# Performance work log

Measured on AMD Instinct MI355X. Metric: run time of the kernel, lower is better.

Reference implementation:

```python
import jax, jax.numpy as jnp
import numpy as np

B, C, W, H = 16, 512, 64, 64
OUT, NH = 512, 8
HD = OUT // NH          # 64
K = 64                  # kernel_size == attended axis length (height)


def setup_inputs() -> dict:
    key = jax.random.key(0)
    k0, k1, k2, k3 = jax.random.split(key, 4)
    s = float(HD) ** -0.5
    return {
        "x": jax.random.normal(k0, (B, C, W, H), jnp.float32),
        "in_proj_weight": jax.random.normal(k1, (2 * OUT, C), jnp.float32) * s,
        "in_proj_bias": jnp.zeros((2 * OUT,), jnp.float32),
        "out_proj_w": jax.random.normal(k2, (OUT, OUT), jnp.float32) * s,
        "out_proj_b": jnp.zeros((OUT,), jnp.float32),
        "relative": jax.random.normal(k3, (2 * HD, 2 * K - 1), jnp.float32) * s,
    }


def reference(x, in_proj_weight, in_proj_bias, out_proj_w, out_proj_b, relative):
    b, c, w, h = x.shape
    hd2 = HD // 2
    # width=False, self-attention path: permute(0,3,2,1) then flat view
    xq = jnp.transpose(x, (0, 3, 2, 1)).reshape(b * w, h, c)
    qkv = xq @ in_proj_weight.T + in_proj_bias
    q, k, v = jnp.split(qkv, [OUT // 2, OUT], axis=2)

    # relative position embeddings gathered into [2*HD, K, K]
    rel_idx = jnp.arange(K)[:, None] - jnp.arange(K)[None, :] + (K - 1)  # key i, query j
    emb = relative[:, rel_idx]                                          # [2*HD, K, K]
    q_emb, k_emb, v_emb = jnp.split(emb, [hd2, HD], axis=0)

    # [bw, heads, ch, pos]
    q = q.reshape(b * w, h, NH, hd2).transpose(0, 2, 3, 1)
    k = k.reshape(b * w, h, NH, hd2).transpose(0, 2, 3, 1)
    v = v.reshape(b * w, h, NH, HD).transpose(0, 2, 3, 1)

    qr = jnp.einsum('bgci,cij->bgij', q, q_emb)
    kr = jnp.einsum('bgci,cij->bgij', k, k_emb).swapaxes(2, 3)
    qk = jnp.einsum('bgci,bgcj->bgij', q, k)
    sim = jax.nn.softmax(qk + qr + kr, axis=3)

    sv = jnp.einsum('bgij,bgcj->bgci', sim, v)     # [bw, NH, HD, h]
    sve = jnp.einsum('bgij,cij->bgci', sim, v_emb)  # [bw, NH, HD, h]
    out = (sv + sve).reshape(b * w, OUT, h).swapaxes(1, 2)  # [bw, h, OUT]
    out = out @ out_proj_w.T + out_proj_b
    # [b, w, h, OUT] -> transpose(2,3) -> permute(0,2,3,1) == transpose(0,3,2,1)
    out = out.reshape(b, w, h, OUT).transpose(0, 3, 2, 1)   # [B, OUT, H, W]
    return out
```

## Files before the change

### kernel.cpp

```cpp
#include <hip/hip_runtime.h>

using u16 = unsigned short;
using u32 = unsigned int;
typedef __attribute__((ext_vector_type(8))) _Float16 h8v;
typedef __attribute__((ext_vector_type(8))) u16 us8;
typedef __attribute__((ext_vector_type(4))) float f4v;

__device__ __forceinline__ u16 f2h(float f) {
  _Float16 h = (_Float16)f;
  return __builtin_bit_cast(unsigned short, h);
}
__device__ __forceinline__ _Float16 bits2h(u16 u) {
  return __builtin_bit_cast(_Float16, u);
}

__device__ __forceinline__ f4v mfma16(h8v a, h8v b, f4v c) {
  return __builtin_amdgcn_mfma_f32_16x16x32_f16(a, b, c, 0, 0, 0);
}

__device__ __forceinline__ void gll16(const void* g, void* l) {
  __builtin_amdgcn_global_load_lds(
      (const __attribute__((address_space(1))) void*)g,
      (__attribute__((address_space(3))) void*)l, 16, 0, 0);
}


__global__ __launch_bounds__(256) void k0_setup(
    const float* __restrict__ w1, const float* __restrict__ wout,
    const float* __restrict__ rel, u16* __restrict__ W1b, u16* __restrict__ Woutb,
    u16* __restrict__ EqT, u16* __restrict__ EkT, u16* __restrict__ Evp)
{
  int idx = blockIdx.x * 256 + threadIdx.x;
  if (idx < 524288) {
    W1b[idx] = f2h(w1[idx]);
  } else if (idx < 786432) {
    int k = idx - 524288; Woutb[k] = f2h(wout[k]);
  } else if (idx < 790528) {
    int k = idx - 786432; int t = k >> 5, c = k & 31;
    EqT[k] = (t < 127) ? f2h(rel[c * 127 + t]) : (u16)0;
  } else if (idx < 794624) {
    int k = idx - 790528; int t = k >> 5, c = k & 31;
    EkT[k] = (t < 127) ? f2h(rel[(32 + c) * 127 + t]) : (u16)0;
  } else if (idx < 802816) {
    int k = idx - 794624; int c = k >> 7, t = k & 127;
    Evp[k] = (t < 127) ? f2h(rel[(64 + c) * 127 + t]) : (u16)0;
  }
}

__global__ __launch_bounds__(256) void k0t_transpose(
    const float* __restrict__ x, u16* __restrict__ xT)
{
  const int bid = blockIdx.x;
  const int cc = bid & 7, w = (bid >> 3) & 63, b = bid >> 9;
  const int c0 = cc * 64;
  const int t = threadIdx.x;
  __shared__ float T[64 * 65];

  const float* xb = x + ((size_t)(b * 512 + c0) * 64 + w) * 64;
#pragma unroll
  for (int p = 0; p < 4; p++) {
    int ci = (t >> 4) + p * 16;
    int pos = (t & 15) * 4;
    float4 v = *(const float4*)&xb[(size_t)ci * 4096 + pos];
    T[ci * 65 + pos + 0] = v.x; T[ci * 65 + pos + 1] = v.y;
    T[ci * 65 + pos + 2] = v.z; T[ci * 65 + pos + 3] = v.w;
  }
  __syncthreads();
  size_t Rb = (size_t)b * 4096 + (size_t)w * 64;
#pragma unroll
  for (int p = 0; p < 2; p++) {
    int u = p * 256 + t;
    int h = u >> 3, ch = u & 7;
    us8 o;
#pragma unroll
    for (int e = 0; e < 8; e++) o[e] = f2h(T[(ch * 8 + e) * 65 + h]);
    *(us8*)&xT[(Rb + h) * 512 + c0 + ch * 8] = o;
  }
}

__global__ __launch_bounds__(512, 1) void k1_qkv(
    const u16* __restrict__ xT, const u16* __restrict__ W1b,
    const float* __restrict__ bias, u16* __restrict__ qkv)
{
  __shared__ u16 POOL[81920];
  u16* XL = POOL;
  u16* Bl = POOL + 65536;
  const int rt = blockIdx.x;
  const int b = rt >> 5, w0 = (rt & 31) * 2;
  const int tid = threadIdx.x;
  const int l = tid & 63, wv = tid >> 6;
  const int lr = l & 15, lg = l >> 4;
  const int osub = (wv & 1) * 64;
  const int rsub = (wv >> 1) * 32;
  const size_t Rbase = (size_t)rt * 128;

#pragma unroll
  for (int i = 0; i < 16; i++) {
    int r = wv * 16 + i;
    gll16(xT + (Rbase + r) * 512 + ((l ^ (r & 7)) << 3), XL + r * 512);
  }

  auto stageB = [&](int ot, int kk, int buf) {
#pragma unroll
    for (int q = 0; q < 2; q++) {
      int slot = q * 512 + tid;
      int o = slot >> 3, c4 = slot & 7;
      gll16(W1b + (size_t)(ot * 128 + o) * 512 + kk * 64 + ((c4 ^ (o & 7)) << 3),
            Bl + buf * 8192 + slot * 8);
    }
  };

  stageB(0, 0, 0);
  __syncthreads();

  for (int ot = 0; ot < 8; ot++) {
    const int o0 = ot * 128;
    f4v acc[4][2];
#pragma unroll
    for (int mt = 0; mt < 4; mt++)
#pragma unroll
      for (int nt = 0; nt < 2; nt++) acc[mt][nt] = (f4v){0.f, 0.f, 0.f, 0.f};

#pragma unroll
    for (int kk = 0; kk < 8; kk++) {
      int cur = kk & 1;
      if (kk < 7) stageB(ot, kk + 1, cur ^ 1);
      h8v wf[4][2], xf[2][2];
#pragma unroll
      for (int mt = 0; mt < 4; mt++)
#pragma unroll
        for (int kc = 0; kc < 2; kc++) {
          int o = osub + mt * 16 + lr;
          wf[mt][kc] = *(const h8v*)&Bl[cur * 8192 + o * 64 +
                                        (((kc * 4 + lg) ^ (o & 7)) << 3)];
        }
#pragma unroll
      for (int nt = 0; nt < 2; nt++)
#pragma unroll
        for (int kc = 0; kc < 2; kc++) {
          int r = rsub + nt * 16 + lr;
          xf[nt][kc] = *(const h8v*)&XL[r * 512 + kk * 64 +
                                        (((kc * 4 + lg) ^ (r & 7)) << 3)];
        }
#pragma unroll
      for (int mt = 0; mt < 4; mt++)
#pragma unroll
        for (int nt = 0; nt < 2; nt++)
#pragma unroll
          for (int kc = 0; kc < 2; kc++)
            acc[mt][nt] = mfma16(wf[mt][kc], xf[nt][kc], acc[mt][nt]);
      __syncthreads();
    }

    u16* Tr = Bl;
#pragma unroll
    for (int mt = 0; mt < 4; mt++)
#pragma unroll
      for (int nt = 0; nt < 2; nt++) {
        int r = rsub + nt * 16 + lr;
#pragma unroll
        for (int ep = 0; ep < 2; ep++) {
          int o_ = osub + mt * 16 + lg * 4 + 2 * ep;
          float v0 = acc[mt][nt][2 * ep + 0] + bias[o0 + o_];
          float v1 = acc[mt][nt][2 * ep + 1] + bias[o0 + o_ + 1];
          unsigned pk = (unsigned)f2h(v0) | ((unsigned)f2h(v1) << 16);
          int cc = o_ >> 3;
          int dst = (cc & 8) | ((cc & 7) ^ (r & 7));
          *(unsigned*)&Tr[r * 128 + dst * 8 + (o_ & 7)] = pk;
        }
      }
    __syncthreads();
#pragma unroll
    for (int p = 0; p < 4; p++) {
      int u = p * 512 + tid;
      int r = u >> 4, cc = u & 15;
      int dst = (cc & 8) | ((cc & 7) ^ (r & 7));
      us8 v = *(const us8*)&Tr[r * 128 + dst * 8];
      int h = r & 63, wl = r >> 6;
      size_t S = (size_t)(b * 64 + h) * 64 + w0 + wl;
      *(us8*)&qkv[S * 1024 + o0 + cc * 8] = v;
    }
    __syncthreads();
    if (ot < 7) { stageB(ot + 1, 0, 0); __syncthreads(); }
  }
}

__global__ __launch_bounds__(256, 4) void k2_attn(
    const u16* __restrict__ qkv, const u16* __restrict__ EqT,
    const u16* __restrict__ EkT, const u16* __restrict__ Evp,
    u16* __restrict__ attn)
{
  const int bid = blockIdx.x;
  const int s = bid >> 3, g = bid & 7;
  const int tid = threadIdx.x;
  const int l = tid & 63, wv = tid >> 6;
  const int lr = l & 15, lg = l >> 4;
  const int i0 = wv * 16;
  const u16* base = qkv + (size_t)s * 65536;

  __shared__ __align__(16) u16 POOL[16896];
  u16* QEt  = POOL;
  u16* KEtT = POOL + 8448;
  u16* Pl   = POOL;
  u16* VTl  = POOL + 4096;
  u16* Psh  = POOL + 8192;

  us8 vreg0, vreg1;
  {
    int u0 = tid,        j0_ = u0 >> 3, cb0 = u0 & 7;
    int u1 = tid + 256,  j1_ = u1 >> 3, cb1 = u1 & 7;
    vreg0 = *(const us8*)(base + j0_ * 1024 + 512 + g * 64 + cb0 * 8);
    vreg1 = *(const us8*)(base + j1_ * 1024 + 512 + g * 64 + cb1 * 8);
  }

  h8v qf = *(const h8v*)(base + (i0 + lr) * 1024 + g * 32 + lg * 8);
  h8v kf[4];
#pragma unroll
  for (int jt = 0; jt < 4; jt++)
    kf[jt] = *(const h8v*)(base + (jt * 16 + lr) * 1024 + 256 + g * 32 + lg * 8);

  const f4v z4 = {0.f, 0.f, 0.f, 0.f};

#pragma unroll
  for (int tt = 0; tt < 8; tt++) {
    h8v eb = *(const h8v*)(EqT + (tt * 16 + lr) * 32 + lg * 8);
    f4v d = mfma16(qf, eb, z4);
#pragma unroll
    for (int p = 0; p < 2; p++) {
      u32 pk = (u32)f2h(d[2 * p]) | ((u32)f2h(d[2 * p + 1]) << 16);
      *(u32*)&QEt[(tt * 16 + lr) * 66 + i0 + lg * 4 + 2 * p] = pk;
    }
  }
#pragma unroll
  for (int q = 0; q < 2; q++) {
    int tt = wv * 2 + q;
    h8v ea = *(const h8v*)(EkT + (tt * 16 + lr) * 32 + lg * 8);
#pragma unroll
    for (int jt = 0; jt < 4; jt++) {
      f4v d = mfma16(ea, kf[jt], z4);
#pragma unroll
      for (int e = 0; e < 4; e++)
        KEtT[(tt * 16 + 4 * lg + e) * 66 + jt * 16 + lr] = f2h(d[e]);
    }
  }
  f4v sc[4];
#pragma unroll
  for (int jt = 0; jt < 4; jt++) sc[jt] = mfma16(qf, kf[jt], z4);

  __syncthreads();

  float pv[4][4];
#pragma unroll
  for (int jt = 0; jt < 4; jt++)
#pragma unroll
    for (int r = 0; r < 4; r++) {
      int i = i0 + lg * 4 + r;
      int j = jt * 16 + lr;
      int tq = i - j + 63;
      pv[jt][r] = sc[jt][r] + (float)bits2h(QEt[tq * 66 + i]) +
                  (float)bits2h(KEtT[(126 - tq) * 66 + j]);
    }
  float rsum[4];
#pragma unroll
  for (int r = 0; r < 4; r++) {
    float m = fmaxf(fmaxf(pv[0][r], pv[1][r]), fmaxf(pv[2][r], pv[3][r]));
    m = fmaxf(m, __shfl_xor(m, 1));
    m = fmaxf(m, __shfl_xor(m, 2));
    m = fmaxf(m, __shfl_xor(m, 4));
    m = fmaxf(m, __shfl_xor(m, 8));
    float t0 = 0.f;
#pragma unroll
    for (int jt = 0; jt < 4; jt++) {
      pv[jt][r] = exp2f((pv[jt][r] - m) * 1.4426950408889634f);
      t0 += pv[jt][r];
    }
    t0 += __shfl_xor(t0, 1);
    t0 += __shfl_xor(t0, 2);
    t0 += __shfl_xor(t0, 4);
    t0 += __shfl_xor(t0, 8);
    rsum[r] = t0;
  }

  __syncthreads();

#pragma unroll
  for (int jt = 0; jt < 4; jt++)
#pragma unroll
    for (int r = 0; r < 4; r++) {
      int i = i0 + lg * 4 + r;
      int j = jt * 16 + lr;
      u16 ph = f2h(pv[jt][r]);
      Pl[i * 64 + (((j >> 3) ^ (i & 7)) << 3) + (j & 7)] = ph;
      int d = i + 63 - j;
      int cd = d >> 3;
      Psh[i * 128 + (((cd & 8) | ((cd & 7) ^ (i & 7))) << 3) + (d & 7)] = ph;
    }
  {
    int zi = tid >> 2;
#pragma unroll
    for (int kk = 0; kk < 16; kk++) {
      int k = (tid & 3) * 16 + kk;
      int col = (k < zi) ? k : (k + 64);
      int cd = col >> 3;
      Psh[zi * 128 + (((cd & 8) | ((cd & 7) ^ (zi & 7))) << 3) + (col & 7)] = 0;
    }
    int u0 = tid, j0_ = u0 >> 3, cb0 = u0 & 7;
#pragma unroll
    for (int e = 0; e < 8; e++) {
      int c = cb0 * 8 + e;
      VTl[c * 64 + (((j0_ >> 3) ^ (c & 7)) << 3) + (j0_ & 7)] = (u16)vreg0[e];
    }
    int u1 = tid + 256, j1_ = u1 >> 3, cb1 = u1 & 7;
#pragma unroll
    for (int e = 0; e < 8; e++) {
      int c = cb1 * 8 + e;
      VTl[c * 64 + (((j1_ >> 3) ^ (c & 7)) << 3) + (j1_ & 7)] = (u16)vreg1[e];
    }
  }
  __syncthreads();

  f4v acc[4] = {z4, z4, z4, z4};
  {
    int i = i0 + lr;
#pragma unroll
    for (int kc = 0; kc < 2; kc++) {
      h8v pa = *(const h8v*)&Pl[i * 64 + (((kc * 4 + lg) ^ (i & 7)) << 3)];
#pragma unroll
      for (int ct = 0; ct < 4; ct++) {
        int cA = ct * 16 + lr;
        h8v vb = *(const h8v*)&VTl[cA * 64 + (((kc * 4 + lg) ^ (cA & 7)) << 3)];
        acc[ct] = mfma16(pa, vb, acc[ct]);
      }
    }
#pragma unroll
    for (int tc = 0; tc < 4; tc++) {
      int cd = tc * 4 + lg;
      int cds = (cd & 8) | ((cd & 7) ^ (i & 7));
      h8v pa = *(const h8v*)&Psh[i * 128 + cds * 8];
#pragma unroll
      for (int ct = 0; ct < 4; ct++) {
        h8v eb = *(const h8v*)(Evp + (ct * 16 + lr) * 128 + tc * 32 + lg * 8);
        acc[ct] = mfma16(pa, eb, acc[ct]);
      }
    }
  }
  float inv[4];
#pragma unroll
  for (int r = 0; r < 4; r++) inv[r] = 1.f / rsum[r];
#pragma unroll
  for (int ct = 0; ct < 4; ct++)
#pragma unroll
    for (int r = 0; r < 4; r++) {
      int i = i0 + lg * 4 + r;
      attn[(size_t)(s * 64 + i) * 512 + g * 64 + ct * 16 + lr] =
          f2h(acc[ct][r] * inv[r]);
    }
}

__global__ __launch_bounds__(512) void k3_oproj(
    const u16* __restrict__ attn, const u16* __restrict__ Woutb,
    const float* __restrict__ ob, float* __restrict__ out)
{
  const int bid = blockIdx.x;
  const int b = bid >> 6, w = bid & 63;
  const int tid = threadIdx.x;
  const int l = tid & 63, wv = tid >> 6;
  const int lr = l & 15, lg = l >> 4;

  __shared__ u16 Bl[2][64 * 64];

  f4v acc[4][4];
#pragma unroll
  for (int a_ = 0; a_ < 4; a_++)
#pragma unroll
    for (int b_ = 0; b_ < 4; b_++) acc[a_][b_] = (f4v){0.f, 0.f, 0.f, 0.f};

  auto stageB = [&](int kk, int buf) {
    int c0 = kk * 64;
    int h_l = wv * 8 + (l >> 3);
    int p = l & 7;
    const u16* src = attn + ((size_t)b * 4096 + (size_t)h_l * 64 + w) * 512 + c0 +
                     ((p ^ (h_l & 7)) << 3);
    gll16(src, &Bl[buf][wv * 512]);
  };

  stageB(0, 0);
  __syncthreads();

  for (int kk = 0; kk < 8; kk++) {
    int cur = kk & 1, nxt = cur ^ 1;
    if (kk < 7) stageB(kk + 1, nxt);
    int c0 = kk * 64;
    h8v af[4][2], bf[4][2];
#pragma unroll
    for (int mt = 0; mt < 4; mt++)
#pragma unroll
      for (int kc = 0; kc < 2; kc++)
        af[mt][kc] = *(const h8v*)(Woutb + (size_t)(wv * 64 + mt * 16 + lr) * 512 +
                                   c0 + kc * 32 + lg * 8);
#pragma unroll
    for (int jt = 0; jt < 4; jt++)
#pragma unroll
      for (int kc = 0; kc < 2; kc++) {
        int h = jt * 16 + lr;
        bf[jt][kc] = *(const h8v*)&Bl[cur][h * 64 + (((kc * 4 + lg) ^ (h & 7)) << 3)];
      }
#pragma unroll
    for (int mt = 0; mt < 4; mt++)
#pragma unroll
      for (int jt = 0; jt < 4; jt++)
#pragma unroll
        for (int kc = 0; kc < 2; kc++)
          acc[mt][jt] = mfma16(af[mt][kc], bf[jt][kc], acc[mt][jt]);
    __syncthreads();
  }

#pragma unroll
  for (int mt = 0; mt < 4; mt++)
#pragma unroll
    for (int jt = 0; jt < 4; jt++)
#pragma unroll
      for (int e = 0; e < 4; e++) {
        int o = wv * 64 + mt * 16 + lg * 4 + e;
        int h = jt * 16 + lr;
        out[(((size_t)b * 512 + o) * 64 + w) * 64 + h] = acc[mt][jt][e] + ob[o];
      }
}

extern "C" void kernel_launch(void* const* d_in, const int* in_sizes, int n_in,
                              void* d_out, int out_size, void* d_ws, size_t ws_size,
                              hipStream_t stream)
{
  (void)in_sizes; (void)n_in; (void)out_size; (void)ws_size;
  const float* x    = (const float*)d_in[0];
  const float* w1   = (const float*)d_in[1];
  const float* b1   = (const float*)d_in[2];
  const float* wout = (const float*)d_in[3];
  const float* bo   = (const float*)d_in[4];
  const float* rel  = (const float*)d_in[5];
  float* out = (float*)d_out;

  char* ws = (char*)d_ws;
  u16* qkv_ws  = (u16*)ws;
  u16* attn_ws = (u16*)(ws + 134217728);
  u16* xT_ws   = attn_ws;
  u16* W1b     = (u16*)(ws + 201326592);
  u16* Woutb   = (u16*)(ws + 202375168);
  u16* EqT     = (u16*)(ws + 202899456);
  u16* EkT     = (u16*)(ws + 202907648);
  u16* Evp     = (u16*)(ws + 202915840);

  k0_setup<<<dim3(3136), dim3(256), 0, stream>>>(w1, wout, rel, W1b, Woutb, EqT, EkT, Evp);
  k0t_transpose<<<dim3(8192), dim3(256), 0, stream>>>(x, xT_ws);
  k1_qkv  <<<dim3(512),  dim3(512), 0, stream>>>(xT_ws, W1b, b1, qkv_ws);
  k2_attn <<<dim3(8192), dim3(256), 0, stream>>>(qkv_ws, EqT, EkT, Evp, attn_ws);
  k3_oproj<<<dim3(1024), dim3(512), 0, stream>>>(attn_ws, Woutb, bo, out);
}
```

Baseline: 344.0 us.

## Transpose attention score tiles so each lane owns one query row

The QK and relative-embedding MFMAs now use swapped operands, so each lane holds scores along one query row. The softmax max and sum then need two cross-lane shuffles instead of four per row. The relative-embedding tables are stored row-major with a stride of 132, written as packed 64-bit stores, and read back through diagonal indexing. Normalization moves before the P stores, the final 1/sum scaling is dropped, and the occupancy hint is removed from launch bounds. This risks changing register pressure and occupancy, and normalizing before the fp16 conversion slightly changes rounding.

```diff
diff --git a/kernel.cpp b/kernel.cpp
--- a/kernel.cpp
+++ b/kernel.cpp
@@ -4,6 +4,7 @@
 using u32 = unsigned int;
 typedef __attribute__((ext_vector_type(8))) _Float16 h8v;
 typedef __attribute__((ext_vector_type(8))) u16 us8;
+typedef __attribute__((ext_vector_type(2))) u32 u32x2;
 typedef __attribute__((ext_vector_type(4))) float f4v;
 
 __device__ __forceinline__ u16 f2h(float f) {
@@ -185,7 +186,7 @@
   }
 }
 
-__global__ __launch_bounds__(256, 4) void k2_attn(
+__global__ __launch_bounds__(256) void k2_attn(
     const u16* __restrict__ qkv, const u16* __restrict__ EqT,
     const u16* __restrict__ EkT, const u16* __restrict__ Evp,
     u16* __restrict__ attn)
@@ -199,11 +200,11 @@
   const u16* base = qkv + (size_t)s * 65536;
 
   __shared__ __align__(16) u16 POOL[16896];
-  u16* QEt  = POOL;
-  u16* KEtT = POOL + 8448;
-  u16* Pl   = POOL;
-  u16* VTl  = POOL + 4096;
-  u16* Psh  = POOL + 8192;
+  u16* QEi = POOL;
+  u16* KEj = POOL + 8448;
+  u16* Pl  = POOL;
+  u16* VTl = POOL + 4096;
+  u16* Psh = POOL + 8192;
 
   us8 vreg0, vreg1;
   {
@@ -224,12 +225,12 @@
 #pragma unroll
   for (int tt = 0; tt < 8; tt++) {
     h8v eb = *(const h8v*)(EqT + (tt * 16 + lr) * 32 + lg * 8);
-    f4v d = mfma16(qf, eb, z4);
-#pragma unroll
-    for (int p = 0; p < 2; p++) {
-      u32 pk = (u32)f2h(d[2 * p]) | ((u32)f2h(d[2 * p + 1]) << 16);
-      *(u32*)&QEt[(tt * 16 + lr) * 66 + i0 + lg * 4 + 2 * p] = pk;
-    }
+    f4v d = mfma16(eb, qf, z4);
+    int tb = tt * 16 + 4 * lg;
+    u32x2 pk;
+    pk[0] = (u32)f2h(d[0]) | ((u32)f2h(d[1]) << 16);
+    pk[1] = (u32)f2h(d[2]) | ((u32)f2h(d[3]) << 16);
+    *(u32x2*)&QEi[(i0 + lr) * 132 + tb] = pk;
   }
 #pragma unroll
   for (int q = 0; q < 2; q++) {
@@ -238,63 +239,77 @@
 #pragma unroll
     for (int jt = 0; jt < 4; jt++) {
       f4v d = mfma16(ea, kf[jt], z4);
-#pragma unroll
-      for (int e = 0; e < 4; e++)
-        KEtT[(tt * 16 + 4 * lg + e) * 66 + jt * 16 + lr] = f2h(d[e]);
+      int tb = tt * 16 + 4 * lg;
+      u32x2 pk;
+      pk[0] = (u32)f2h(d[0]) | ((u32)f2h(d[1]) << 16);
+      pk[1] = (u32)f2h(d[2]) | ((u32)f2h(d[3]) << 16);
+      *(u32x2*)&KEj[(jt * 16 + lr) * 132 + tb] = pk;
     }
   }
   f4v sc[4];
 #pragma unroll
-  for (int jt = 0; jt < 4; jt++) sc[jt] = mfma16(qf, kf[jt], z4);
-
-  __syncthreads();
-
+  for (int jt = 0; jt < 4; jt++) sc[jt] = mfma16(kf[jt], qf, z4);
+
+  __syncthreads();
+
+  const int i = i0 + lr;
   float pv[4][4];
+  {
+    int qbase = i * 133 + 63 - 4 * lg;
+    int kbase = 8448 + 4 * lg * 133 + 63 - i;
+#pragma unroll
+    for (int jt = 0; jt < 4; jt++)
+#pragma unroll
+      for (int e = 0; e < 4; e++) {
+        float qr = (float)bits2h(POOL[qbase - 16 * jt - e]);
+        float kr = (float)bits2h(POOL[kbase + 2128 * jt + 133 * e]);
+        pv[jt][e] = sc[jt][e] + qr + kr;
+      }
+  }
+  float inv;
+  {
+    float m = pv[0][0];
+#pragma unroll
+    for (int jt = 0; jt < 4; jt++)
+#pragma unroll
+      for (int e = 0; e < 4; e++) m = fmaxf(m, pv[jt][e]);
+    m = fmaxf(m, __shfl_xor(m, 16));
+    m = fmaxf(m, __shfl_xor(m, 32));
+    float t0 = 0.f;
+#pragma unroll
+    for (int jt = 0; jt < 4; jt++)
+#pragma unroll
+      for (int e = 0; e < 4; e++) {
+        pv[jt][e] = exp2f((pv[jt][e] - m) * 1.4426950408889634f);
+        t0 += pv[jt][e];
+      }
+    t0 += __shfl_xor(t0, 16);
+    t0 += __shfl_xor(t0, 32);
+    inv = 1.f / t0;
+  }
 #pragma unroll
   for (int jt = 0; jt < 4; jt++)
 #pragma unroll
-    for (int r = 0; r < 4; r++) {
-      int i = i0 + lg * 4 + r;
-      int j = jt * 16 + lr;
-      int tq = i - j + 63;
-      pv[jt][r] = sc[jt][r] + (float)bits2h(QEt[tq * 66 + i]) +
-                  (float)bits2h(KEtT[(126 - tq) * 66 + j]);
-    }
-  float rsum[4];
-#pragma unroll
-  for (int r = 0; r < 4; r++) {
-    float m = fmaxf(fmaxf(pv[0][r], pv[1][r]), fmaxf(pv[2][r], pv[3][r]));
-    m = fmaxf(m, __shfl_xor(m, 1));
-    m = fmaxf(m, __shfl_xor(m, 2));
-    m = fmaxf(m, __shfl_xor(m, 4));
-    m = fmaxf(m, __shfl_xor(m, 8));
-    float t0 = 0.f;
-#pragma unroll
-    for (int jt = 0; jt < 4; jt++) {
-      pv[jt][r] = exp2f((pv[jt][r] - m) * 1.4426950408889634f);
-      t0 += pv[jt][r];
-    }
-    t0 += __shfl_xor(t0, 1);
-    t0 += __shfl_xor(t0, 2);
-    t0 += __shfl_xor(t0, 4);
-    t0 += __shfl_xor(t0, 8);
-    rsum[r] = t0;
-  }
-
-  __syncthreads();
-
-#pragma unroll
-  for (int jt = 0; jt < 4; jt++)
-#pragma unroll
-    for (int r = 0; r < 4; r++) {
-      int i = i0 + lg * 4 + r;
-      int j = jt * 16 + lr;
-      u16 ph = f2h(pv[jt][r]);
-      Pl[i * 64 + (((j >> 3) ^ (i & 7)) << 3) + (j & 7)] = ph;
-      int d = i + 63 - j;
+    for (int e = 0; e < 4; e++) pv[jt][e] *= inv;
+
+  __syncthreads();
+
+#pragma unroll
+  for (int jt = 0; jt < 4; jt++) {
+    int j0 = jt * 16 + 4 * lg;
+    int jc = j0 >> 3;
+    u32x2 pk;
+    pk[0] = (u32)f2h(pv[jt][0]) | ((u32)f2h(pv[jt][1]) << 16);
+    pk[1] = (u32)f2h(pv[jt][2]) | ((u32)f2h(pv[jt][3]) << 16);
+    *(u32x2*)&Pl[i * 64 + ((jc ^ (i & 7)) << 3) + (j0 & 7)] = pk;
+#pragma unroll
+    for (int e = 0; e < 4; e++) {
+      int d = i + 63 - (j0 + e);
       int cd = d >> 3;
-      Psh[i * 128 + (((cd & 8) | ((cd & 7) ^ (i & 7))) << 3) + (d & 7)] = ph;
-    }
+      Psh[i * 128 + (((cd & 8) | ((cd & 7) ^ (i & 7))) << 3) + (d & 7)] =
+          f2h(pv[jt][e]);
+    }
+  }
   {
     int zi = tid >> 2;
 #pragma unroll
@@ -321,7 +336,6 @@
 
   f4v acc[4] = {z4, z4, z4, z4};
   {
-    int i = i0 + lr;
 #pragma unroll
     for (int kc = 0; kc < 2; kc++) {
       h8v pa = *(const h8v*)&Pl[i * 64 + (((kc * 4 + lg) ^ (i & 7)) << 3)];
@@ -344,16 +358,12 @@
       }
     }
   }
-  float inv[4];
-#pragma unroll
-  for (int r = 0; r < 4; r++) inv[r] = 1.f / rsum[r];
 #pragma unroll
   for (int ct = 0; ct < 4; ct++)
 #pragma unroll
     for (int r = 0; r < 4; r++) {
-      int i = i0 + lg * 4 + r;
-      attn[(size_t)(s * 64 + i) * 512 + g * 64 + ct * 16 + lr] =
-          f2h(acc[ct][r] * inv[r]);
+      int io = i0 + lg * 4 + r;
+      attn[(size_t)(s * 64 + io) * 512 + g * 64 + ct * 16 + lr] = f2h(acc[ct][r]);
     }
 }
 
```

Measured after the change: 337.9 us. Within noise of the previous version (-1.8%).
